# Kernel tuning notes

Hardware: AMD Instinct MI355X
Metric: run time of the kernel (lower is better)

## Reference

```python
import jax, jax.numpy as jnp
import numpy as np

NUM_LEVELS = 4
RADIUS = 3
B, H, W, C = 2, 64, 64, 64
N = 4096


def _bilinear_sample(feat, coords):
    # feat: (B, H, W, C); coords: (B, N, 2) in [0,W-1]x[0,H-1]
    Bf, Hf, Wf, Cf = feat.shape
    x = coords[..., 0]
    y = coords[..., 1]
    x0 = jnp.clip(jnp.floor(x).astype(jnp.int32), 0, Wf - 1)
    x1 = jnp.clip(jnp.floor(x).astype(jnp.int32) + 1, 0, Wf - 1)
    y0 = jnp.clip(jnp.floor(y).astype(jnp.int32), 0, Hf - 1)
    y1 = jnp.clip(jnp.floor(y).astype(jnp.int32) + 1, 0, Hf - 1)
    # weights use the CLIPPED corner coords (matches original code order)
    wa = (x1.astype(jnp.float32) - x) * (y1.astype(jnp.float32) - y)
    wb = (x1.astype(jnp.float32) - x) * (y - y0.astype(jnp.float32))
    wc = (x - x0.astype(jnp.float32)) * (y1.astype(jnp.float32) - y)
    wd = (x - x0.astype(jnp.float32)) * (y - y0.astype(jnp.float32))
    bidx = jnp.arange(Bf)[:, None]
    Ia = feat[bidx, y0, x0, :]
    Ib = feat[bidx, y1, x0, :]
    Ic = feat[bidx, y0, x1, :]
    Id = feat[bidx, y1, x1, :]
    return (wa[..., None] * Ia + wb[..., None] * Ib
            + wc[..., None] * Ic + wd[..., None] * Id)


def _build_pyramid(fmap2):
    # pyramid holds L2-normalized fmap2 at successively halved resolutions
    f = fmap2 / (jnp.linalg.norm(fmap2, axis=-1, keepdims=True) + 1e-6)
    pyr = [f]
    cur = f
    for level in range(NUM_LEVELS - 1):
        cur = jax.image.resize(
            cur, (B, H // 2 ** (level + 1), W // 2 ** (level + 1), C),
            method='bilinear')
        pyr.append(cur)
    return pyr


def _corr_block(fmap1, fmap2, coords):
    r = RADIUS
    # fmap1 is normalized in the original but its result is unused; replicate faithfully
    _ = fmap1 / (jnp.linalg.norm(fmap1, axis=-1, keepdims=True) + 1e-6)
    pyramid = _build_pyramid(fmap2)
    # (dx, dy) offsets, dy outer / dx inner to match original concat order
    offsets = jnp.array([[dx, dy] for dy in range(-r, r + 1)
                         for dx in range(-r, r + 1)], dtype=jnp.float32)  # (K,2)
    K = offsets.shape[0]
    outs = []
    for level, corr in enumerate(pyramid):
        scale = 2 ** level
        H_l, W_l = corr.shape[1], corr.shape[2]
        coords_scaled = coords / scale                       # (B,N,2)
        coords_off = coords_scaled[None] + offsets[:, None, None, :]  # (K,B,N,2)
        coords_off = jnp.clip(coords_off,
                              jnp.array([0.0, 0.0]),
                              jnp.array([W_l - 1, H_l - 1], dtype=jnp.float32))
        sampled = jax.vmap(_bilinear_sample, in_axes=(None, 0))(corr, coords_off)  # (K,B,N,C)
        outs.append(jnp.moveaxis(sampled, 0, 2).reshape(coords.shape[0], coords.shape[1], K * corr.shape[-1]))
    return jnp.concatenate(outs, axis=-1)  # (B, N, NUM_LEVELS*K*C)


def setup_inputs() -> dict:
    key = jax.random.key(0)
    k1, k2, k3 = jax.random.split(key, 3)
    fmap1 = jax.random.normal(k1, (B, H, W, C), dtype=jnp.float32)
    fmap2 = jax.random.normal(k2, (B, H, W, C), dtype=jnp.float32)
    coords = jax.random.uniform(k3, (B, N, 2), dtype=jnp.float32) \
        * jnp.array([W - 1, H - 1], dtype=jnp.float32)
    return {"fmap1": fmap1, "fmap2": fmap2, "coords": coords}


def reference(fmap1, fmap2, coords):
    return _corr_block(fmap1, fmap2, coords)
```

## Files before the change

### kernel.cpp

```cpp
#include <hip/hip_runtime.h>
#include <math.h>


__global__ __launch_bounds__(256) void normalize_kernel(
    const float* __restrict__ in, float* __restrict__ out) {
  int gtid = blockIdx.x * 256 + threadIdx.x;
  int wave = gtid >> 6;
  int lane = gtid & 63;
  float v = in[wave * 64 + lane];
  float ss = v * v;
  #pragma unroll
  for (int m = 32; m >= 1; m >>= 1) ss += __shfl_xor(ss, m);
  out[wave * 64 + lane] = v / (sqrtf(ss) + 1e-6f);
}

__global__ __launch_bounds__(256) void downsample_kernel(
    const float* __restrict__ in, float* __restrict__ out, int Si) {
  int So = Si >> 1;
  int gtid = blockIdx.x * 256 + threadIdx.x;
  int wave = gtid >> 6;
  int lane = gtid & 63;
  int ox = wave % So;
  int t  = wave / So;
  int oy = t % So;
  int b  = t / So;

  int xs[4], ys[4];
  float wx[4], wy[4];
  float bw[4] = {0.25f, 0.75f, 0.75f, 0.25f};
  float sx = 0.f, sy = 0.f;
  #pragma unroll
  for (int tt = 0; tt < 4; tt++) {
    int jx = 2 * ox - 1 + tt;
    bool vx = (jx >= 0) && (jx < Si);
    xs[tt] = vx ? jx : 0;
    wx[tt] = vx ? bw[tt] : 0.f;
    sx += wx[tt];
    int jy = 2 * oy - 1 + tt;
    bool vy = (jy >= 0) && (jy < Si);
    ys[tt] = vy ? jy : 0;
    wy[tt] = vy ? bw[tt] : 0.f;
    sy += wy[tt];
  }
  float ix = 1.f / sx, iy = 1.f / sy;
  #pragma unroll
  for (int tt = 0; tt < 4; tt++) { wx[tt] *= ix; wy[tt] *= iy; }

  float acc = 0.f;
  #pragma unroll
  for (int a = 0; a < 4; a++) {
    const float* rp = in + ((long)(b * Si + ys[a]) * Si) * 64 + lane;
    float row = 0.f;
    #pragma unroll
    for (int tt = 0; tt < 4; tt++) row += wx[tt] * rp[xs[tt] * 64];
    acc += wy[a] * row;
  }
  out[((long)(b * So + oy) * So + ox) * 64 + lane] = acc;
}

__global__ __launch_bounds__(448, 4) void corr_sample_reg(
    const float* __restrict__ pyr, const float* __restrict__ coords,
    float* __restrict__ out) {
  unsigned bn = blockIdx.x;
  unsigned b  = bn >> 12;
  int t   = threadIdx.x;
  int c4  = t & 15;
  int g   = t >> 4;
  int l   = g & 3;
  int dyi = g >> 2;

  int Wl = 64 >> l;
  float sc  = 1.0f / (float)(1 << l);
  float fmx = (float)(Wl - 1);
  unsigned base4 = (524288u - (524288u >> (2 * l))) / 3u;

  float cx = coords[bn * 2 + 0];
  float cy = coords[bn * 2 + 1];
  float cxs = cx * sc, cys = cy * sc;

  float y = fminf(fmaxf(cys + (float)(dyi - 3), 0.f), fmx);
  int y0 = (int)floorf(y);
  int y1 = min(y0 + 1, Wl - 1);
  float wy0 = (float)y1 - y;
  float wy1 = y - (float)y0;

  const float4* p4 = (const float4*)pyr;
  unsigned pixb = (unsigned)(b * Wl * Wl);
  unsigned r0 = base4 + ((pixb + (unsigned)(y0 * Wl)) << 4) + (unsigned)c4;
  unsigned r1 = base4 + ((pixb + (unsigned)(y1 * Wl)) << 4) + (unsigned)c4;

  unsigned ob = bn * 3136u + (unsigned)l * 784u + ((unsigned)(dyi * 7) << 4) + (unsigned)c4;
  float4* o4 = (float4*)out;

  int px = -1;
  float4 a0 = make_float4(0.f, 0.f, 0.f, 0.f), a1 = a0;
  #pragma unroll
  for (int dxi = 0; dxi < 7; ++dxi) {
    float x = fminf(fmaxf(cxs + (float)(dxi - 3), 0.f), fmx);
    int x0 = (int)floorf(x);
    int x1 = min(x0 + 1, Wl - 1);
    float wx0 = (float)x1 - x;
    float wx1 = x - (float)x0;

    float4 b0, b1;
    if (x0 == px) { b0 = a0; b1 = a1; }
    else { b0 = p4[r0 + ((unsigned)x0 << 4)]; b1 = p4[r1 + ((unsigned)x0 << 4)]; }
    a0 = p4[r0 + ((unsigned)x1 << 4)];
    a1 = p4[r1 + ((unsigned)x1 << 4)];
    px = x1;

    float4 r;
    r.x = wx0 * (wy0 * b0.x + wy1 * b1.x) + wx1 * (wy0 * a0.x + wy1 * a1.x);
    r.y = wx0 * (wy0 * b0.y + wy1 * b1.y) + wx1 * (wy0 * a0.y + wy1 * a1.y);
    r.z = wx0 * (wy0 * b0.z + wy1 * b1.z) + wx1 * (wy0 * a0.z + wy1 * a1.z);
    r.w = wx0 * (wy0 * b0.w + wy1 * b1.w) + wx1 * (wy0 * a0.w + wy1 * a1.w);
    o4[ob + (unsigned)(dxi << 4)] = r;
  }
}

extern "C" void kernel_launch(void* const* d_in, const int* in_sizes, int n_in,
                              void* d_out, int out_size, void* d_ws, size_t ws_size,
                              hipStream_t stream) {
  const float* fmap2  = (const float*)d_in[1];
  const float* coords = (const float*)d_in[2];
  float* out = (float*)d_out;
  float* pyr = (float*)d_ws;

  normalize_kernel<<<2048, 256, 0, stream>>>(fmap2, pyr);
  downsample_kernel<<<512, 256, 0, stream>>>(pyr,          pyr + 524288, 64);
  downsample_kernel<<<128, 256, 0, stream>>>(pyr + 524288, pyr + 655360, 32);
  downsample_kernel<<< 32, 256, 0, stream>>>(pyr + 655360, pyr + 688128, 16);
  corr_sample_reg<<<8192, 448, 0, stream>>>(pyr, coords, out);
}
```

Baseline: 86.91 us.

## Fuse pyramid downsampling into one kernel and use nontemporal output stores

Replaces three dependent downsample launches with a single kernel that computes levels 1-3 directly from level 0. It does this by composing the bilinear tap weights into wider 10- and 22-tap filters, which removes two launches and their serialization. It also changes the thread-to-(level,dy) mapping in the sampler to l = g/7 and writes output with nontemporal stores to avoid cache pollution. The cost is far more gather work per output for the coarse levels, and floating-point summation order changes slightly.

```diff
diff --git a/kernel.cpp b/kernel.cpp
--- a/kernel.cpp
+++ b/kernel.cpp
@@ -1,6 +1,8 @@
 #include <hip/hip_runtime.h>
 #include <math.h>
 
+
+typedef float f32x4 __attribute__((ext_vector_type(4)));
 
 __global__ __launch_bounds__(256) void normalize_kernel(
     const float* __restrict__ in, float* __restrict__ out) {
@@ -14,63 +16,114 @@
   out[wave * 64 + lane] = v / (sqrtf(ss) + 1e-6f);
 }
 
-__global__ __launch_bounds__(256) void downsample_kernel(
-    const float* __restrict__ in, float* __restrict__ out, int Si) {
-  int So = Si >> 1;
-  int gtid = blockIdx.x * 256 + threadIdx.x;
-  int wave = gtid >> 6;
-  int lane = gtid & 63;
-  int ox = wave % So;
-  int t  = wave / So;
-  int oy = t % So;
-  int b  = t / So;
+__device__ __forceinline__ void taps4(int i, int S_in, float (&w)[4]) {
+  float s = 0.f;
+  #pragma unroll
+  for (int t = 0; t < 4; t++) {
+    int j = 2 * i - 1 + t;
+    float bw = (t == 0 || t == 3) ? 0.25f : 0.75f;
+    w[t] = (j >= 0 && j < S_in) ? bw : 0.f;
+    s += w[t];
+  }
+  float inv = 1.f / s;
+  #pragma unroll
+  for (int t = 0; t < 4; t++) w[t] *= inv;
+}
 
-  int xs[4], ys[4];
-  float wx[4], wy[4];
-  float bw[4] = {0.25f, 0.75f, 0.75f, 0.25f};
-  float sx = 0.f, sy = 0.f;
+template <int N>
+__device__ __forceinline__ void expand_taps(int jlo, const float (&win)[N],
+                                            int S_in, float (&wout)[2 * N + 2]) {
   #pragma unroll
-  for (int tt = 0; tt < 4; tt++) {
-    int jx = 2 * ox - 1 + tt;
-    bool vx = (jx >= 0) && (jx < Si);
-    xs[tt] = vx ? jx : 0;
-    wx[tt] = vx ? bw[tt] : 0.f;
-    sx += wx[tt];
-    int jy = 2 * oy - 1 + tt;
-    bool vy = (jy >= 0) && (jy < Si);
-    ys[tt] = vy ? jy : 0;
-    wy[tt] = vy ? bw[tt] : 0.f;
-    sy += wy[tt];
+  for (int t = 0; t < 2 * N + 2; t++) wout[t] = 0.f;
+  #pragma unroll
+  for (int t = 0; t < N; t++) {
+    int i = jlo + t;
+    float w4[4];
+    float s = 0.f;
+    #pragma unroll
+    for (int u = 0; u < 4; u++) {
+      int j = 2 * i - 1 + u;
+      float bw = (u == 0 || u == 3) ? 0.25f : 0.75f;
+      w4[u] = (j >= 0 && j < S_in) ? bw : 0.f;
+      s += w4[u];
+    }
+    float inv = (win[t] != 0.f) ? win[t] / s : 0.f;
+    #pragma unroll
+    for (int u = 0; u < 4; u++) wout[2 * t + u] += w4[u] * inv;
   }
-  float ix = 1.f / sx, iy = 1.f / sy;
-  #pragma unroll
-  for (int tt = 0; tt < 4; tt++) { wx[tt] *= ix; wy[tt] *= iy; }
+}
 
+template <int NT>
+__device__ __forceinline__ float gather2d(const float* __restrict__ L0n, int b,
+                                          int ch, int ylo, int xlo,
+                                          const float (&wy)[NT],
+                                          const float (&wx)[NT]) {
   float acc = 0.f;
   #pragma unroll
-  for (int a = 0; a < 4; a++) {
-    const float* rp = in + ((long)(b * Si + ys[a]) * Si) * 64 + lane;
-    float row = 0.f;
-    #pragma unroll
-    for (int tt = 0; tt < 4; tt++) row += wx[tt] * rp[xs[tt] * 64];
-    acc += wy[a] * row;
+  for (int a = 0; a < NT; a++) {
+    if (wy[a] != 0.f) {
+      int jy = min(max(ylo + a, 0), 63);
+      const float* row = L0n + (((b * 64 + jy) * 64) << 6) + ch;
+      float racc = 0.f;
+      #pragma unroll
+      for (int t = 0; t < NT; t++) {
+        int jx = min(max(xlo + t, 0), 63);
+        racc += wx[t] * row[jx << 6];
+      }
+      acc += wy[a] * racc;
+    }
   }
-  out[((long)(b * So + oy) * So + ox) * 64 + lane] = acc;
+  return acc;
+}
+
+__global__ __launch_bounds__(256) void levels_kernel(
+    const float* __restrict__ pyr_in, float* __restrict__ pyr_out) {
+  int gtid = blockIdx.x * 256 + threadIdx.x;
+  int ch = gtid & 63;
+  int px = gtid >> 6;
+  if (px < 2048) {
+    int b = px >> 10, r = px & 1023, oy = r >> 5, ox = r & 31;
+    float wy[4], wx[4];
+    taps4(oy, 64, wy);
+    taps4(ox, 64, wx);
+    float v = gather2d<4>(pyr_in, b, ch, 2 * oy - 1, 2 * ox - 1, wy, wx);
+    pyr_out[524288 + ((((b * 32 + oy) * 32 + ox)) << 6) + ch] = v;
+  } else if (px < 2560) {
+    int p = px - 2048, b = p >> 8, r = p & 255, oy = r >> 4, ox = r & 15;
+    float t4[4], wy[10], wx[10];
+    taps4(oy, 32, t4);
+    expand_taps<4>(2 * oy - 1, t4, 64, wy);
+    taps4(ox, 32, t4);
+    expand_taps<4>(2 * ox - 1, t4, 64, wx);
+    float v = gather2d<10>(pyr_in, b, ch, 4 * oy - 3, 4 * ox - 3, wy, wx);
+    pyr_out[655360 + ((((b * 16 + oy) * 16 + ox)) << 6) + ch] = v;
+  } else {
+    int p = px - 2560, b = p >> 6, r = p & 63, oy = r >> 3, ox = r & 7;
+    float t4[4], t10[10], wy[22], wx[22];
+    taps4(oy, 16, t4);
+    expand_taps<4>(2 * oy - 1, t4, 32, t10);
+    expand_taps<10>(4 * oy - 3, t10, 64, wy);
+    taps4(ox, 16, t4);
+    expand_taps<4>(2 * ox - 1, t4, 32, t10);
+    expand_taps<10>(4 * ox - 3, t10, 64, wx);
+    float v = gather2d<22>(pyr_in, b, ch, 8 * oy - 7, 8 * ox - 7, wy, wx);
+    pyr_out[688128 + ((((b * 8 + oy) * 8 + ox)) << 6) + ch] = v;
+  }
 }
 
 __global__ __launch_bounds__(448, 4) void corr_sample_reg(
     const float* __restrict__ pyr, const float* __restrict__ coords,
     float* __restrict__ out) {
   unsigned bn = blockIdx.x;
-  unsigned b  = bn >> 12;
-  int t   = threadIdx.x;
-  int c4  = t & 15;
-  int g   = t >> 4;
-  int l   = g & 3;
-  int dyi = g >> 2;
+  unsigned b = bn >> 12;
+  int t = threadIdx.x;
+  int c4 = t & 15;
+  int g = t >> 4;
+  int l = g / 7;
+  int dyi = g - l * 7;
 
   int Wl = 64 >> l;
-  float sc  = 1.0f / (float)(1 << l);
+  float sc = 1.0f / (float)(1 << l);
   float fmx = (float)(Wl - 1);
   unsigned base4 = (524288u - (524288u >> (2 * l))) / 3u;
 
@@ -89,8 +142,9 @@
   unsigned r0 = base4 + ((pixb + (unsigned)(y0 * Wl)) << 4) + (unsigned)c4;
   unsigned r1 = base4 + ((pixb + (unsigned)(y1 * Wl)) << 4) + (unsigned)c4;
 
-  unsigned ob = bn * 3136u + (unsigned)l * 784u + ((unsigned)(dyi * 7) << 4) + (unsigned)c4;
-  float4* o4 = (float4*)out;
+  unsigned ob = bn * 3136u + (unsigned)l * 784u + ((unsigned)(dyi * 7) << 4) +
+                (unsigned)c4;
+  f32x4* o4 = (f32x4*)out;
 
   int px = -1;
   float4 a0 = make_float4(0.f, 0.f, 0.f, 0.f), a1 = a0;
@@ -103,32 +157,34 @@
     float wx1 = x - (float)x0;
 
     float4 b0, b1;
-    if (x0 == px) { b0 = a0; b1 = a1; }
-    else { b0 = p4[r0 + ((unsigned)x0 << 4)]; b1 = p4[r1 + ((unsigned)x0 << 4)]; }
+    if (x0 == px) {
+      b0 = a0; b1 = a1;
+    } else {
+      b0 = p4[r0 + ((unsigned)x0 << 4)];
+      b1 = p4[r1 + ((unsigned)x0 << 4)];
+    }
     a0 = p4[r0 + ((unsigned)x1 << 4)];
     a1 = p4[r1 + ((unsigned)x1 << 4)];
     px = x1;
 
-    float4 r;
+    f32x4 r;
     r.x = wx0 * (wy0 * b0.x + wy1 * b1.x) + wx1 * (wy0 * a0.x + wy1 * a1.x);
     r.y = wx0 * (wy0 * b0.y + wy1 * b1.y) + wx1 * (wy0 * a0.y + wy1 * a1.y);
     r.z = wx0 * (wy0 * b0.z + wy1 * b1.z) + wx1 * (wy0 * a0.z + wy1 * a1.z);
     r.w = wx0 * (wy0 * b0.w + wy1 * b1.w) + wx1 * (wy0 * a0.w + wy1 * a1.w);
-    o4[ob + (unsigned)(dxi << 4)] = r;
+    __builtin_nontemporal_store(r, o4 + ob + (unsigned)(dxi << 4));
   }
 }
 
 extern "C" void kernel_launch(void* const* d_in, const int* in_sizes, int n_in,
                               void* d_out, int out_size, void* d_ws, size_t ws_size,
                               hipStream_t stream) {
-  const float* fmap2  = (const float*)d_in[1];
+  const float* fmap2 = (const float*)d_in[1];
   const float* coords = (const float*)d_in[2];
   float* out = (float*)d_out;
   float* pyr = (float*)d_ws;
 
   normalize_kernel<<<2048, 256, 0, stream>>>(fmap2, pyr);
-  downsample_kernel<<<512, 256, 0, stream>>>(pyr,          pyr + 524288, 64);
-  downsample_kernel<<<128, 256, 0, stream>>>(pyr + 524288, pyr + 655360, 32);
-  downsample_kernel<<< 32, 256, 0, stream>>>(pyr + 655360, pyr + 688128, 16);
+  levels_kernel<<<672, 256, 0, stream>>>(pyr, pyr);
   corr_sample_reg<<<8192, 448, 0, stream>>>(pyr, coords, out);
 }
```

Result: slower. 100.3 us (+15.5%).
